# Kernel optimization log

Measured on AMD Instinct MI355X. Metric: run time of the kernel, lower is better.

Reference implementation:

```python
import jax, jax.numpy as jnp
import numpy as np

N = 2_000_000
WIDTH, HEIGHT = 1920, 1080
ZNEAR, ZFAR = 0.01, 100.0
TAN_FOVX = 0.5773503  # 60 deg horizontal FoV
TAN_FOVY = TAN_FOVX * HEIGHT / WIDTH


def _camera():
    # Row-vector convention: x_view = x_h @ world2view (translation in last row).
    w2v = np.eye(4, dtype=np.float32)
    w2v[3, 2] = 5.0  # push scene 5 units in front of the camera
    P = np.zeros((4, 4), dtype=np.float32)
    P[0, 0] = 1.0 / TAN_FOVX
    P[1, 1] = 1.0 / TAN_FOVY
    P[2, 2] = ZFAR / (ZFAR - ZNEAR)
    P[3, 2] = -(ZFAR * ZNEAR) / (ZFAR - ZNEAR)
    P[2, 3] = 1.0
    full = w2v @ P
    return jnp.asarray(w2v), jnp.asarray(full)


def setup_inputs() -> dict:
    key = jax.random.key(0)
    ks = jax.random.split(key, 5)
    w2v, full = _camera()
    return dict(
        points=jax.random.normal(ks[0], (N, 3), jnp.float32) * 2.0,
        colors=jax.random.uniform(ks[1], (N, 3), jnp.float32),
        opacity=jax.random.normal(ks[2], (N,), jnp.float32),
        scales=jax.random.uniform(ks[3], (N, 3), jnp.float32, minval=0.01, maxval=0.2),
        quaternions=jax.random.normal(ks[4], (N, 4), jnp.float32),
        world2view=w2v,
        full_proj_transform=full,
        tan_fovX=jnp.full((1,), TAN_FOVX, jnp.float32),
        tan_fovY=jnp.full((1,), TAN_FOVY, jnp.float32),
        focal_x=jnp.full((1,), WIDTH / (2.0 * TAN_FOVX), jnp.float32),
        focal_y=jnp.full((1,), HEIGHT / (2.0 * TAN_FOVY), jnp.float32),
        width=WIDTH,
        height=HEIGHT,
    )


def _quat_to_rot(q):
    q = q / jnp.linalg.norm(q, axis=-1, keepdims=True)
    w, x, y, z = q[:, 0], q[:, 1], q[:, 2], q[:, 3]
    R = jnp.stack([
        1 - 2 * (y * y + z * z), 2 * (x * y - w * z), 2 * (x * z + w * y),
        2 * (x * y + w * z), 1 - 2 * (x * x + z * z), 2 * (y * z - w * x),
        2 * (x * z - w * y), 2 * (y * z + w * x), 1 - 2 * (x * x + y * y),
    ], axis=-1)
    return R.reshape(-1, 3, 3)


def reference(points, colors, opacity, scales, quaternions, world2view,
              full_proj_transform, tan_fovX, tan_fovY, focal_x, focal_y,
              width, height):
    n = points.shape[0]
    # --- 3D covariance: Sigma = (R S)(R S)^T ---
    R = _quat_to_rot(quaternions)                      # [N,3,3]
    M = R * scales[:, None, :]                         # R @ diag(s)
    cov3d = jnp.einsum('nij,nkj->nik', M, M)           # [N,3,3]

    # --- view / clip transforms (row-vector convention) ---
    ph = jnp.concatenate([points, jnp.ones((n, 1), points.dtype)], axis=1)
    pview = ph @ world2view                            # [N,4]
    zview = pview[:, 2]
    in_view = zview >= 0.2                             # frustum (near-plane) cull

    pclip = ph @ full_proj_transform
    pndc = pclip[:, :3] / pclip[:, 3:4]
    px = ((pndc[:, 0] + 1.0) * width - 1.0) * 0.5      # ndc2Pix
    py = ((pndc[:, 1] + 1.0) * height - 1.0) * 0.5

    # --- 2D covariance via projection Jacobian (EWA splatting) ---
    xc = jnp.clip(pview[:, 0] / zview, -1.3 * tan_fovX, 1.3 * tan_fovX) * zview
    yc = jnp.clip(pview[:, 1] / zview, -1.3 * tan_fovY, 1.3 * tan_fovY) * zview
    z2 = zview * zview
    zero = jnp.zeros_like(zview)
    J = jnp.stack([
        focal_x / zview, zero, -(focal_x * xc) / z2,
        zero, focal_y / zview, -(focal_y * yc) / z2,
        zero, zero, zero,
    ], axis=-1).reshape(-1, 3, 3)                      # [N,3,3]
    W = world2view[:3, :3].T
    T = jnp.einsum('nij,jk->nik', J, W)
    cov2d = jnp.einsum('nij,njk,nlk->nil', T, cov3d, T)[:, :2, :2]

    # --- analytic 2x2 inverse ---
    c00, c01 = cov2d[:, 0, 0], cov2d[:, 0, 1]
    c10, c11 = cov2d[:, 1, 0], cov2d[:, 1, 1]
    det = c00 * c11 - c01 * c10
    det_safe = jnp.where(jnp.abs(det) < 1e-6, 1e-6, det)
    inv_cov = jnp.stack([c11, -c01, -c10, c00], axis=-1) / det_safe[:, None]

    # --- extent / radius: 3 sigma of dominant eigenvalue ---
    mid = 0.5 * (c00 + c11)
    inter = jnp.maximum(mid * mid - det, 0.1)
    lam = mid + jnp.sqrt(inter)
    radius = jnp.ceil(3.0 * jnp.sqrt(jnp.maximum(lam, 0.0)))

    min_x = jnp.floor(px - radius)
    min_y = jnp.floor(py - radius)
    max_x = jnp.ceil(px + radius)
    max_y = jnp.ceil(py + radius)

    # --- depth sort; culled gaussians keyed to +inf (fixed-shape stand-in for boolean gather) ---
    depth_key = jnp.where(in_view, zview, jnp.float32(jnp.inf))
    order = jnp.argsort(depth_key)

    packed = jnp.concatenate([
        px[:, None], py[:, None], zview[:, None],
        cov2d.reshape(n, 4), inv_cov,
        radius[:, None],
        min_x[:, None], min_y[:, None], max_x[:, None], max_y[:, None],
        colors, jax.nn.sigmoid(opacity)[:, None],
        in_view.astype(points.dtype)[:, None],
    ], axis=1)                                          # [N,21]
    return packed[order]
```

## Files before the change

kernel.cpp:

```cpp
#include <hip/hip_runtime.h>
#include <hip/hip_bf16.h>
#include <math.h>

#define BLK   256
#define IPT   16
#define TILE  (BLK * IPT)
#define CHUNK 1024
#define BINS  256
#define PASSES 4
#define SCT   4096

__global__ __launch_bounds__(256) void k_rows(const float* __restrict__ pts,
                                              const float* __restrict__ cols,
                                              const float* __restrict__ opa,
                                              const float* __restrict__ scl,
                                              const float* __restrict__ qt,
                                              const float* __restrict__ w2v,
                                              const float* __restrict__ fpm,
                                              const float* __restrict__ tanx_p,
                                              const float* __restrict__ tany_p,
                                              const float* __restrict__ fx_p,
                                              const float* __restrict__ fy_p,
                                              const int* __restrict__ wp,
                                              const int* __restrict__ hp,
                                              float* __restrict__ rows,
                                              unsigned* __restrict__ keys,
                                              int N)
{
    int i = blockIdx.x * 256 + threadIdx.x;
    if (i >= N) return;

    float x = pts[3*i+0], y = pts[3*i+1], z = pts[3*i+2];

    float zv = x*w2v[2] + y*w2v[6] + z*w2v[10] + w2v[14];
    bool in_view = (zv >= 0.2f);
    {
        float key = in_view ? zv : __int_as_float(0x7f800000);
        unsigned u = __float_as_uint(key);
        u ^= (u & 0x80000000u) ? 0xFFFFFFFFu : 0x80000000u;
        keys[i] = u;
    }

    float4 q4 = *(const float4*)(qt + 4*i);
    float qw = q4.x, qx = q4.y, qy = q4.z, qz = q4.w;
    float rn = __builtin_amdgcn_rsqf(qw*qw + qx*qx + qy*qy + qz*qz);
    qw *= rn; qx *= rn; qy *= rn; qz *= rn;
    float R00 = 1.f - 2.f*(qy*qy + qz*qz), R01 = 2.f*(qx*qy - qw*qz), R02 = 2.f*(qx*qz + qw*qy);
    float R10 = 2.f*(qx*qy + qw*qz), R11 = 1.f - 2.f*(qx*qx + qz*qz), R12 = 2.f*(qy*qz - qw*qx);
    float R20 = 2.f*(qx*qz - qw*qy), R21 = 2.f*(qy*qz + qw*qx), R22 = 1.f - 2.f*(qx*qx + qy*qy);

    float s0 = scl[3*i+0], s1 = scl[3*i+1], s2 = scl[3*i+2];
    float M00=R00*s0, M01=R01*s1, M02=R02*s2;
    float M10=R10*s0, M11=R11*s1, M12=R12*s2;
    float M20=R20*s0, M21=R21*s1, M22=R22*s2;
    float C00=M00*M00+M01*M01+M02*M02;
    float C01=M00*M10+M01*M11+M02*M12;
    float C02=M00*M20+M01*M21+M02*M22;
    float C11=M10*M10+M11*M11+M12*M12;
    float C12=M10*M20+M11*M21+M12*M22;
    float C22=M20*M20+M21*M21+M22*M22;

    float pvx = x*w2v[0] + y*w2v[4] + z*w2v[8]  + w2v[12];
    float pvy = x*w2v[1] + y*w2v[5] + z*w2v[9]  + w2v[13];

    float cx = x*fpm[0] + y*fpm[4] + z*fpm[8]  + fpm[12];
    float cy = x*fpm[1] + y*fpm[5] + z*fpm[9]  + fpm[13];
    float cw = x*fpm[3] + y*fpm[7] + z*fpm[11] + fpm[15];
    float rcw = __builtin_amdgcn_rcpf(cw);
    float Wf = (float)wp[0], Hf = (float)hp[0];
    float px = ((cx*rcw + 1.f) * Wf - 1.f) * 0.5f;
    float py = ((cy*rcw + 1.f) * Hf - 1.f) * 0.5f;

    float tanX = tanx_p[0], tanY = tany_p[0], fx = fx_p[0], fy = fy_p[0];
    float lx = 1.3f * tanX, ly = 1.3f * tanY;
    float rzv = __builtin_amdgcn_rcpf(zv);
    float xc = fminf(fmaxf(pvx*rzv, -lx), lx) * zv;
    float yc = fminf(fmaxf(pvy*rzv, -ly), ly) * zv;
    float rz2 = rzv * rzv;
    float J00 = fx * rzv, J02 = -(fx * xc) * rz2;
    float J11 = fy * rzv, J12 = -(fy * yc) * rz2;

    float T00 = J00*w2v[0] + J02*w2v[2];
    float T01 = J00*w2v[4] + J02*w2v[6];
    float T02 = J00*w2v[8] + J02*w2v[10];
    float T10 = J11*w2v[1] + J12*w2v[2];
    float T11 = J11*w2v[5] + J12*w2v[6];
    float T12 = J11*w2v[9] + J12*w2v[10];

    float V00 = T00*C00 + T01*C01 + T02*C02;
    float V01 = T00*C01 + T01*C11 + T02*C12;
    float V02 = T00*C02 + T01*C12 + T02*C22;
    float V10 = T10*C00 + T11*C01 + T12*C02;
    float V11 = T10*C01 + T11*C11 + T12*C12;
    float V12 = T10*C02 + T11*C12 + T12*C22;
    float c00 = V00*T00 + V01*T01 + V02*T02;
    float c01 = V00*T10 + V01*T11 + V02*T12;
    float c10 = V10*T00 + V11*T01 + V12*T02;
    float c11 = V10*T10 + V11*T11 + V12*T12;

    float det = c00*c11 - c01*c10;
    float det_safe = (fabsf(det) < 1e-6f) ? 1e-6f : det;
    float rdet = __builtin_amdgcn_rcpf(det_safe);
    float i00 =  c11 * rdet, i01 = -c01 * rdet, i11 = c00 * rdet;
    float mid = 0.5f * (c00 + c11);
    float inter = fmaxf(mid*mid - det, 0.1f);
    float lam = mid + sqrtf(inter);
    float radius = ceilf(3.0f * sqrtf(fmaxf(lam, 0.0f)));
    float op = __builtin_amdgcn_rcpf(1.0f + __expf(-opa[i]));

    float cr = cols[3*i+0], cg = cols[3*i+1], cb = cols[3*i+2];

    float4* rp = (float4*)(rows + (size_t)i * 16);
    rp[0] = make_float4(px,  py,  zv,  c00);
    rp[1] = make_float4(c01, c11, i00, i01);
    rp[2] = make_float4(i11, radius, cr, cg);
    rp[3] = make_float4(cb,  op,  in_view ? 1.0f : 0.0f, 0.f);
}

__global__ __launch_bounds__(256) void k_hist8(const unsigned* __restrict__ keys,
                                               int N, int numTiles, int shift,
                                               unsigned* __restrict__ hist)
{
    __shared__ unsigned hb[4][BINS];
    int t = threadIdx.x, b = blockIdx.x, w = t >> 6;
    hb[0][t] = 0; hb[1][t] = 0; hb[2][t] = 0; hb[3][t] = 0;
    __syncthreads();
    int base = b * TILE + t * 16;
    if (base + 16 <= N) {
        const uint4* p = (const uint4*)(keys + base);
        #pragma unroll
        for (int q = 0; q < 4; ++q) {
            uint4 v = p[q];
            atomicAdd(&hb[w][(v.x >> shift) & 255u], 1u);
            atomicAdd(&hb[w][(v.y >> shift) & 255u], 1u);
            atomicAdd(&hb[w][(v.z >> shift) & 255u], 1u);
            atomicAdd(&hb[w][(v.w >> shift) & 255u], 1u);
        }
    } else {
        for (int k = 0; k < 16; ++k) {
            int i = base + k;
            if (i < N) atomicAdd(&hb[w][(keys[i] >> shift) & 255u], 1u);
        }
    }
    __syncthreads();
    hist[t * numTiles + b] = hb[0][t] + hb[1][t] + hb[2][t] + hb[3][t];
}

__global__ __launch_bounds__(256) void k_scanA(const unsigned* __restrict__ h, int E,
                                               unsigned* __restrict__ bsum)
{
    __shared__ unsigned red[256];
    int t = threadIdx.x;
    int base = blockIdx.x * SCT + t * 16;
    unsigned acc = 0;
    if (base + 16 <= E) {
        const uint4* p = (const uint4*)(h + base);
        #pragma unroll
        for (int q = 0; q < 4; ++q) { uint4 v = p[q]; acc += v.x + v.y + v.z + v.w; }
    } else {
        for (int k = 0; k < 16; ++k) { int i = base + k; if (i < E) acc += h[i]; }
    }
    red[t] = acc;
    __syncthreads();
    for (int off = 128; off > 0; off >>= 1) {
        if (t < off) red[t] += red[t + off];
        __syncthreads();
    }
    if (t == 0) bsum[blockIdx.x] = red[0];
}

__global__ __launch_bounds__(256) void k_scanB(unsigned* __restrict__ h, int E,
                                               const unsigned* __restrict__ bsum)
{
    __shared__ unsigned tsum[256];
    __shared__ unsigned boff_s;
    int t = threadIdx.x, b = blockIdx.x;
    int base = b * SCT + t * 16;

    if (t == 0) { unsigned o = 0; for (int i = 0; i < b; ++i) o += bsum[i]; boff_s = o; }

    unsigned v[16];
    bool full = (base + 16 <= E);
    if (full) {
        const uint4* p = (const uint4*)(h + base);
        #pragma unroll
        for (int q = 0; q < 4; ++q) { uint4 u = p[q]; v[4*q]=u.x; v[4*q+1]=u.y; v[4*q+2]=u.z; v[4*q+3]=u.w; }
    } else {
        for (int k = 0; k < 16; ++k) { int i = base + k; v[k] = (i < E) ? h[i] : 0u; }
    }
    unsigned acc = 0;
    #pragma unroll
    for (int k = 0; k < 16; ++k) { unsigned x = v[k]; v[k] = acc; acc += x; }
    tsum[t] = acc;
    __syncthreads();
    for (int off = 1; off < 256; off <<= 1) {
        unsigned u = (t >= off) ? tsum[t - off] : 0u;
        __syncthreads();
        tsum[t] += u;
        __syncthreads();
    }
    unsigned add = boff_s + ((t == 0) ? 0u : tsum[t - 1]);
    if (full) {
        uint4* p = (uint4*)(h + base);
        #pragma unroll
        for (int q = 0; q < 4; ++q)
            p[q] = make_uint4(v[4*q] + add, v[4*q+1] + add, v[4*q+2] + add, v[4*q+3] + add);
    } else {
        for (int k = 0; k < 16; ++k) { int i = base + k; if (i < E) h[i] = v[k] + add; }
    }
}

__global__ __launch_bounds__(256) void k_scatter8(const unsigned* __restrict__ keys,
                                                  const unsigned* __restrict__ vals,
                                                  int N, int numTiles, int shift,
                                                  const unsigned* __restrict__ hist,
                                                  unsigned* __restrict__ okeys,
                                                  unsigned* __restrict__ ovals)
{
    __shared__ unsigned short wcnt[4][BINS];
    __shared__ unsigned digStartL[BINS];
    __shared__ unsigned tileBase[BINS];
    __shared__ unsigned tscan[BINS];
    __shared__ unsigned stage[TILE];

    int t = threadIdx.x, b = blockIdx.x;
    int w = t >> 6, l = t & 63;
    int base = b * TILE;
    int nvalid = N - base; if (nvalid < 0) nvalid = 0; if (nvalid > TILE) nvalid = TILE;
    int wbase = base + w * CHUNK;

    ((unsigned*)wcnt)[t] = 0; ((unsigned*)wcnt)[256 + t] = 0;
    __syncthreads();

    unsigned k_[IPT];
    unsigned short rw_[IPT];
    unsigned char d_[IPT];

    #pragma unroll
    for (int it = 0; it < IPT; ++it) {
        int e = wbase + it * 64 + l;
        bool ok = e < N;
        unsigned kk = ok ? keys[e] : 0u;
        unsigned d = (kk >> shift) & 255u;
        unsigned long long mm = __ballot(ok);
        #pragma unroll
        for (int bb = 0; bb < 8; ++bb) {
            unsigned long long bal = __ballot(ok && ((d >> bb) & 1u));
            mm &= ((d >> bb) & 1u) ? bal : ~bal;
        }
        unsigned long long below = mm & ((1ull << l) - 1ull);
        unsigned rk = (unsigned)__popcll(below);
        unsigned before = (unsigned)wcnt[w][d];
        if (ok && rk == 0)
            wcnt[w][d] = (unsigned short)(before + (unsigned)__popcll(mm));
        k_[it]  = kk;
        rw_[it] = (unsigned short)(before + rk);
        d_[it]  = (unsigned char)d;
    }
    __syncthreads();

    {
        unsigned c0 = wcnt[0][t], c1 = wcnt[1][t], c2 = wcnt[2][t], c3 = wcnt[3][t];
        wcnt[0][t] = 0;
        wcnt[1][t] = (unsigned short)c0;
        wcnt[2][t] = (unsigned short)(c0 + c1);
        wcnt[3][t] = (unsigned short)(c0 + c1 + c2);
        tscan[t] = c0 + c1 + c2 + c3;
        tileBase[t] = hist[t * numTiles + b];
    }
    __syncthreads();
    for (int off = 1; off < 256; off <<= 1) {
        unsigned u = (t >= off) ? tscan[t - off] : 0u;
        __syncthreads();
        tscan[t] += u;
        __syncthreads();
    }
    digStartL[t] = (t == 0) ? 0u : tscan[t - 1];
    __syncthreads();

    unsigned lp_[IPT];
    #pragma unroll
    for (int it = 0; it < IPT; ++it) {
        int e = wbase + it * 64 + l;
        if (e < N) {
            unsigned d = d_[it];
            lp_[it] = digStartL[d] + (unsigned)wcnt[w][d] + (unsigned)rw_[it];
            stage[lp_[it]] = k_[it];
        }
    }
    __syncthreads();

    unsigned pos_[IPT];
    #pragma unroll
    for (int it = 0; it < IPT; ++it) {
        int p = it * BLK + t;
        if (p < nvalid) {
            unsigned kk = stage[p];
            unsigned d = (kk >> shift) & 255u;
            unsigned pos = tileBase[d] + ((unsigned)p - digStartL[d]);
            pos_[it] = pos;
            if (okeys) okeys[pos] = kk;
        }
    }
    __syncthreads();

    #pragma unroll
    for (int it = 0; it < IPT; ++it) {
        int e = wbase + it * 64 + l;
        if (e < N) stage[lp_[it]] = vals ? vals[e] : (unsigned)e;
    }
    __syncthreads();
    #pragma unroll
    for (int it = 0; it < IPT; ++it) {
        int p = it * BLK + t;
        if (p < nvalid) ovals[pos_[it]] = stage[p];
    }
}

__global__ __launch_bounds__(256) void k_perm(const unsigned* __restrict__ order,
                                              const float* __restrict__ rows,
                                              float* __restrict__ out, int N)
{
    __shared__ float srow[256 * 21];
    int i = blockIdx.x * 256 + threadIdx.x;
    if (i < N) {
        int j = (int)order[i];
        const float4* rp = (const float4*)(rows + (size_t)j * 16);
        float4 a = rp[0], b4 = rp[1], c4 = rp[2], d4 = rp[3];
        float px = a.x,  py = a.y,  zv = a.z,  c00 = a.w;
        float c01 = b4.x, c11 = b4.y, i00 = b4.z, i01 = b4.w;
        float i11 = c4.x, rad = c4.y, cr = c4.z, cg = c4.w;
        float cb = d4.x,  op = d4.y,  iv = d4.z;
        float* r = &srow[threadIdx.x * 21];
        r[0]=px; r[1]=py; r[2]=zv;
        r[3]=c00; r[4]=c01; r[5]=c01; r[6]=c11;
        r[7]=i00; r[8]=i01; r[9]=i01; r[10]=i11;
        r[11]=rad;
        r[12]=floorf(px - rad); r[13]=floorf(py - rad);
        r[14]=ceilf(px + rad);  r[15]=ceilf(py + rad);
        r[16]=cr; r[17]=cg; r[18]=cb;
        r[19]=op; r[20]=iv;
    }
    __syncthreads();
    int blockBase = blockIdx.x * 256;
    int valid = N - blockBase; if (valid > 256) valid = 256;
    if (valid > 0) {
        float* dst = out + (size_t)blockBase * 21;
        for (int u = threadIdx.x; u < valid * 21; u += 256) dst[u] = srow[u];
    }
}

extern "C" void kernel_launch(void* const* d_in, const int* in_sizes, int n_in,
                              void* d_out, int out_size, void* d_ws, size_t ws_size,
                              hipStream_t stream)
{
    const float* pts  = (const float*)d_in[0];
    const float* cols = (const float*)d_in[1];
    const float* opa  = (const float*)d_in[2];
    const float* scl  = (const float*)d_in[3];
    const float* qt   = (const float*)d_in[4];
    const float* w2v  = (const float*)d_in[5];
    const float* fpm  = (const float*)d_in[6];
    const float* tanx = (const float*)d_in[7];
    const float* tany = (const float*)d_in[8];
    const float* fx   = (const float*)d_in[9];
    const float* fy   = (const float*)d_in[10];
    const int*   wp   = (const int*)d_in[11];
    const int*   hp   = (const int*)d_in[12];

    int N = in_sizes[0] / 3;
    int numTiles = (N + TILE - 1) / TILE;
    int nb = (N + 255) / 256;
    int E = BINS * numTiles;
    int nScan = (E + SCT - 1) / SCT;

    unsigned* kA   = (unsigned*)d_ws;
    unsigned* kB   = kA + N;
    unsigned* vA   = kB + N;
    unsigned* vB   = vA + N;
    unsigned* hist = vB + N;
    unsigned* bsum = hist + E;
    float*    rows = (float*)(bsum + nScan);

    k_rows<<<nb, 256, 0, stream>>>(pts, cols, opa, scl, qt, w2v, fpm,
                                   tanx, tany, fx, fy, wp, hp, rows, kA, N);

    k_hist8<<<numTiles, 256, 0, stream>>>(kA, N, numTiles, 0, hist);
    k_scanA<<<nScan, 256, 0, stream>>>(hist, E, bsum);
    k_scanB<<<nScan, 256, 0, stream>>>(hist, E, bsum);
    k_scatter8<<<numTiles, 256, 0, stream>>>(kA, nullptr, N, numTiles, 0, hist, kB, vA);

    k_hist8<<<numTiles, 256, 0, stream>>>(kB, N, numTiles, 8, hist);
    k_scanA<<<nScan, 256, 0, stream>>>(hist, E, bsum);
    k_scanB<<<nScan, 256, 0, stream>>>(hist, E, bsum);
    k_scatter8<<<numTiles, 256, 0, stream>>>(kB, vA, N, numTiles, 8, hist, kA, vB);

    k_hist8<<<numTiles, 256, 0, stream>>>(kA, N, numTiles, 16, hist);
    k_scanA<<<nScan, 256, 0, stream>>>(hist, E, bsum);
    k_scanB<<<nScan, 256, 0, stream>>>(hist, E, bsum);
    k_scatter8<<<numTiles, 256, 0, stream>>>(kA, vB, N, numTiles, 16, hist, kB, vA);

    k_hist8<<<numTiles, 256, 0, stream>>>(kB, N, numTiles, 24, hist);
    k_scanA<<<nScan, 256, 0, stream>>>(hist, E, bsum);
    k_scanB<<<nScan, 256, 0, stream>>>(hist, E, bsum);
    k_scatter8<<<numTiles, 256, 0, stream>>>(kB, vA, N, numTiles, 24, hist, nullptr, vB);

    k_perm<<<nb, 256, 0, stream>>>(vB, rows, (float*)d_out, N);
}
```

Measured before the change: 503.4 us.

## Replace per-pass histogram/scan with one-sweep histogram and decoupled look-back scatter

Computes all four 8-bit digit histograms in a single pass over the keys, using wave-level match aggregation, then scans them in one small kernel. Each scatter pass then derives its per-tile digit offsets with a decoupled look-back over tile states. Tiles are ordered by an atomic ticket so that waiting on predecessors is safe. This removes three histogram passes and eight scan launches, plus the per-tile histogram traffic. In exchange it adds a zeroing kernel and spin-waiting between tiles.

```diff
diff --git a/kernel.cpp b/kernel.cpp
--- a/kernel.cpp
+++ b/kernel.cpp
@@ -1,14 +1,22 @@
 #include <hip/hip_runtime.h>
-#include <hip/hip_bf16.h>
 #include <math.h>
 
 #define BLK   256
 #define IPT   16
-#define TILE  (BLK * IPT)
+#define TILE  4096
 #define CHUNK 1024
 #define BINS  256
-#define PASSES 4
-#define SCT   4096
+
+#define FLAG_AGG (1u << 30)
+#define FLAG_PRE (2u << 30)
+#define VALMASK  0x3FFFFFFFu
+
+__global__ __launch_bounds__(256) void k_zero(unsigned* __restrict__ p, int n)
+{
+    int i = blockIdx.x * 256 + threadIdx.x;
+    int T = gridDim.x * 256;
+    for (; i < n; i += T) p[i] = 0;
+}
 
 __global__ __launch_bounds__(256) void k_rows(const float* __restrict__ pts,
                                               const float* __restrict__ cols,
@@ -117,120 +125,96 @@
     rp[3] = make_float4(cb,  op,  in_view ? 1.0f : 0.0f, 0.f);
 }
 
-__global__ __launch_bounds__(256) void k_hist8(const unsigned* __restrict__ keys,
-                                               int N, int numTiles, int shift,
-                                               unsigned* __restrict__ hist)
+__global__ __launch_bounds__(256) void k_hist_all(const unsigned* __restrict__ keys,
+                                                  int N, unsigned* __restrict__ gh)
 {
     __shared__ unsigned hb[4][BINS];
-    int t = threadIdx.x, b = blockIdx.x, w = t >> 6;
+    int t = threadIdx.x, l = t & 63;
     hb[0][t] = 0; hb[1][t] = 0; hb[2][t] = 0; hb[3][t] = 0;
     __syncthreads();
-    int base = b * TILE + t * 16;
-    if (base + 16 <= N) {
-        const uint4* p = (const uint4*)(keys + base);
+
+    int gtid = blockIdx.x * 256 + t;
+    int T = gridDim.x * 256;
+    int M4 = N >> 2;
+    for (int i = gtid; i < M4; i += T) {
+        uint4 v = ((const uint4*)keys)[i];
+        unsigned ks[4] = {v.x, v.y, v.z, v.w};
         #pragma unroll
-        for (int q = 0; q < 4; ++q) {
-            uint4 v = p[q];
-            atomicAdd(&hb[w][(v.x >> shift) & 255u], 1u);
-            atomicAdd(&hb[w][(v.y >> shift) & 255u], 1u);
-            atomicAdd(&hb[w][(v.z >> shift) & 255u], 1u);
-            atomicAdd(&hb[w][(v.w >> shift) & 255u], 1u);
-        }
-    } else {
-        for (int k = 0; k < 16; ++k) {
-            int i = base + k;
-            if (i < N) atomicAdd(&hb[w][(keys[i] >> shift) & 255u], 1u);
-        }
-    }
-    __syncthreads();
-    hist[t * numTiles + b] = hb[0][t] + hb[1][t] + hb[2][t] + hb[3][t];
-}
-
-__global__ __launch_bounds__(256) void k_scanA(const unsigned* __restrict__ h, int E,
-                                               unsigned* __restrict__ bsum)
-{
-    __shared__ unsigned red[256];
+        for (int c = 0; c < 4; ++c) {
+            unsigned kk = ks[c];
+            #pragma unroll
+            for (int p = 0; p < 4; ++p) {
+                unsigned d = (kk >> (8*p)) & 255u;
+                unsigned long long mm = __ballot(true);
+                #pragma unroll
+                for (int bb = 0; bb < 8; ++bb) {
+                    unsigned long long bal = __ballot(((d >> bb) & 1u) != 0u);
+                    mm &= ((d >> bb) & 1u) ? bal : ~bal;
+                }
+                unsigned long long below = mm & ((1ull << l) - 1ull);
+                if (below == 0ull)
+                    atomicAdd(&hb[p][d], (unsigned)__popcll(mm));
+            }
+        }
+    }
+    if (gtid == 0) {
+        for (int i = M4 << 2; i < N; ++i) {
+            unsigned kk = keys[i];
+            for (int p = 0; p < 4; ++p) atomicAdd(&hb[p][(kk >> (8*p)) & 255u], 1u);
+        }
+    }
+    __syncthreads();
+    #pragma unroll
+    for (int p = 0; p < 4; ++p)
+        if (hb[p][t]) atomicAdd(&gh[p * BINS + t], hb[p][t]);
+}
+
+__global__ __launch_bounds__(256) void k_scan_all(unsigned* __restrict__ gh)
+{
+    __shared__ unsigned tsum[BINS];
     int t = threadIdx.x;
-    int base = blockIdx.x * SCT + t * 16;
-    unsigned acc = 0;
-    if (base + 16 <= E) {
-        const uint4* p = (const uint4*)(h + base);
-        #pragma unroll
-        for (int q = 0; q < 4; ++q) { uint4 v = p[q]; acc += v.x + v.y + v.z + v.w; }
-    } else {
-        for (int k = 0; k < 16; ++k) { int i = base + k; if (i < E) acc += h[i]; }
-    }
-    red[t] = acc;
-    __syncthreads();
-    for (int off = 128; off > 0; off >>= 1) {
-        if (t < off) red[t] += red[t + off];
+    for (int p = 0; p < 4; ++p) {
+        tsum[t] = gh[p * BINS + t];
         __syncthreads();
-    }
-    if (t == 0) bsum[blockIdx.x] = red[0];
-}
-
-__global__ __launch_bounds__(256) void k_scanB(unsigned* __restrict__ h, int E,
-                                               const unsigned* __restrict__ bsum)
-{
-    __shared__ unsigned tsum[256];
-    __shared__ unsigned boff_s;
-    int t = threadIdx.x, b = blockIdx.x;
-    int base = b * SCT + t * 16;
-
-    if (t == 0) { unsigned o = 0; for (int i = 0; i < b; ++i) o += bsum[i]; boff_s = o; }
-
-    unsigned v[16];
-    bool full = (base + 16 <= E);
-    if (full) {
-        const uint4* p = (const uint4*)(h + base);
-        #pragma unroll
-        for (int q = 0; q < 4; ++q) { uint4 u = p[q]; v[4*q]=u.x; v[4*q+1]=u.y; v[4*q+2]=u.z; v[4*q+3]=u.w; }
-    } else {
-        for (int k = 0; k < 16; ++k) { int i = base + k; v[k] = (i < E) ? h[i] : 0u; }
-    }
-    unsigned acc = 0;
-    #pragma unroll
-    for (int k = 0; k < 16; ++k) { unsigned x = v[k]; v[k] = acc; acc += x; }
-    tsum[t] = acc;
-    __syncthreads();
-    for (int off = 1; off < 256; off <<= 1) {
-        unsigned u = (t >= off) ? tsum[t - off] : 0u;
+        for (int off = 1; off < 256; off <<= 1) {
+            unsigned u = (t >= off) ? tsum[t - off] : 0u;
+            __syncthreads();
+            tsum[t] += u;
+            __syncthreads();
+        }
+        unsigned excl = (t == 0) ? 0u : tsum[t - 1];
         __syncthreads();
-        tsum[t] += u;
+        gh[p * BINS + t] = excl;
         __syncthreads();
     }
-    unsigned add = boff_s + ((t == 0) ? 0u : tsum[t - 1]);
-    if (full) {
-        uint4* p = (uint4*)(h + base);
-        #pragma unroll
-        for (int q = 0; q < 4; ++q)
-            p[q] = make_uint4(v[4*q] + add, v[4*q+1] + add, v[4*q+2] + add, v[4*q+3] + add);
-    } else {
-        for (int k = 0; k < 16; ++k) { int i = base + k; if (i < E) h[i] = v[k] + add; }
-    }
-}
-
-__global__ __launch_bounds__(256) void k_scatter8(const unsigned* __restrict__ keys,
-                                                  const unsigned* __restrict__ vals,
-                                                  int N, int numTiles, int shift,
-                                                  const unsigned* __restrict__ hist,
-                                                  unsigned* __restrict__ okeys,
-                                                  unsigned* __restrict__ ovals)
+}
+
+__global__ __launch_bounds__(256) void k_scatter_lb(const unsigned* __restrict__ keys,
+                                                    const unsigned* __restrict__ vals,
+                                                    int N, int shift,
+                                                    const unsigned* __restrict__ gbase,
+                                                    unsigned* __restrict__ tstate,
+                                                    unsigned* __restrict__ ticket,
+                                                    unsigned* __restrict__ okeys,
+                                                    unsigned* __restrict__ ovals)
 {
     __shared__ unsigned short wcnt[4][BINS];
     __shared__ unsigned digStartL[BINS];
     __shared__ unsigned tileBase[BINS];
     __shared__ unsigned tscan[BINS];
     __shared__ unsigned stage[TILE];
-
-    int t = threadIdx.x, b = blockIdx.x;
+    __shared__ unsigned vt_s;
+
+    int t = threadIdx.x;
+    if (t == 0) vt_s = atomicAdd(ticket, 1u);
+    ((unsigned*)wcnt)[t] = 0; ((unsigned*)wcnt)[256 + t] = 0;
+    __syncthreads();
+
+    int b = (int)vt_s;
     int w = t >> 6, l = t & 63;
     int base = b * TILE;
     int nvalid = N - base; if (nvalid < 0) nvalid = 0; if (nvalid > TILE) nvalid = TILE;
     int wbase = base + w * CHUNK;
-
-    ((unsigned*)wcnt)[t] = 0; ((unsigned*)wcnt)[256 + t] = 0;
-    __syncthreads();
 
     unsigned k_[IPT];
     unsigned short rw_[IPT];
@@ -259,14 +243,17 @@
     }
     __syncthreads();
 
+    unsigned own;
     {
         unsigned c0 = wcnt[0][t], c1 = wcnt[1][t], c2 = wcnt[2][t], c3 = wcnt[3][t];
         wcnt[0][t] = 0;
         wcnt[1][t] = (unsigned short)c0;
         wcnt[2][t] = (unsigned short)(c0 + c1);
         wcnt[3][t] = (unsigned short)(c0 + c1 + c2);
-        tscan[t] = c0 + c1 + c2 + c3;
-        tileBase[t] = hist[t * numTiles + b];
+        own = c0 + c1 + c2 + c3;
+        tscan[t] = own;
+        __hip_atomic_store(&tstate[(size_t)b * BINS + t], FLAG_AGG | own,
+                           __ATOMIC_RELEASE, __HIP_MEMORY_SCOPE_AGENT);
     }
     __syncthreads();
     for (int off = 1; off < 256; off <<= 1) {
@@ -276,6 +263,25 @@
         __syncthreads();
     }
     digStartL[t] = (t == 0) ? 0u : tscan[t - 1];
+
+    {
+        unsigned sum = 0;
+        int p = b - 1;
+        while (p >= 0) {
+            unsigned s;
+            do {
+                s = __hip_atomic_load(&tstate[(size_t)p * BINS + t],
+                                      __ATOMIC_RELAXED, __HIP_MEMORY_SCOPE_AGENT);
+                if ((s >> 30) == 0u) __builtin_amdgcn_s_sleep(1);
+            } while ((s >> 30) == 0u);
+            sum += s & VALMASK;
+            if (s & FLAG_PRE) break;
+            --p;
+        }
+        tileBase[t] = gbase[t] + sum;
+        __hip_atomic_store(&tstate[(size_t)b * BINS + t], FLAG_PRE | (sum + own),
+                           __ATOMIC_RELEASE, __HIP_MEMORY_SCOPE_AGENT);
+    }
     __syncthreads();
 
     unsigned lp_[IPT];
@@ -371,39 +377,33 @@
     int N = in_sizes[0] / 3;
     int numTiles = (N + TILE - 1) / TILE;
     int nb = (N + 255) / 256;
-    int E = BINS * numTiles;
-    int nScan = (E + SCT - 1) / SCT;
-
-    unsigned* kA   = (unsigned*)d_ws;
-    unsigned* kB   = kA + N;
-    unsigned* vA   = kB + N;
-    unsigned* vB   = vA + N;
-    unsigned* hist = vB + N;
-    unsigned* bsum = hist + E;
-    float*    rows = (float*)(bsum + nScan);
-
+
+    unsigned* kA     = (unsigned*)d_ws;
+    unsigned* kB     = kA + N;
+    unsigned* vA     = kB + N;
+    unsigned* vB     = vA + N;
+    unsigned* gh     = vB + N;
+    unsigned* tick   = gh + 4 * BINS;
+    unsigned* tstate = tick + 4;
+    float*    rows   = (float*)(tstate + (size_t)4 * numTiles * BINS);
+
+    int zwords = 4 * BINS + 4 + 4 * numTiles * BINS;
+    int zb = (zwords + 255) / 256; if (zb > 1024) zb = 1024;
+
+    k_zero<<<zb, 256, 0, stream>>>(gh, zwords);
     k_rows<<<nb, 256, 0, stream>>>(pts, cols, opa, scl, qt, w2v, fpm,
                                    tanx, tany, fx, fy, wp, hp, rows, kA, N);
-
-    k_hist8<<<numTiles, 256, 0, stream>>>(kA, N, numTiles, 0, hist);
-    k_scanA<<<nScan, 256, 0, stream>>>(hist, E, bsum);
-    k_scanB<<<nScan, 256, 0, stream>>>(hist, E, bsum);
-    k_scatter8<<<numTiles, 256, 0, stream>>>(kA, nullptr, N, numTiles, 0, hist, kB, vA);
-
-    k_hist8<<<numTiles, 256, 0, stream>>>(kB, N, numTiles, 8, hist);
-    k_scanA<<<nScan, 256, 0, stream>>>(hist, E, bsum);
-    k_scanB<<<nScan, 256, 0, stream>>>(hist, E, bsum);
-    k_scatter8<<<numTiles, 256, 0, stream>>>(kB, vA, N, numTiles, 8, hist, kA, vB);
-
-    k_hist8<<<numTiles, 256, 0, stream>>>(kA, N, numTiles, 16, hist);
-    k_scanA<<<nScan, 256, 0, stream>>>(hist, E, bsum);
-    k_scanB<<<nScan, 256, 0, stream>>>(hist, E, bsum);
-    k_scatter8<<<numTiles, 256, 0, stream>>>(kA, vB, N, numTiles, 16, hist, kB, vA);
-
-    k_hist8<<<numTiles, 256, 0, stream>>>(kB, N, numTiles, 24, hist);
-    k_scanA<<<nScan, 256, 0, stream>>>(hist, E, bsum);
-    k_scanB<<<nScan, 256, 0, stream>>>(hist, E, bsum);
-    k_scatter8<<<numTiles, 256, 0, stream>>>(kB, vA, N, numTiles, 24, hist, nullptr, vB);
+    k_hist_all<<<512, 256, 0, stream>>>(kA, N, gh);
+    k_scan_all<<<1, 256, 0, stream>>>(gh);
+
+    k_scatter_lb<<<numTiles, 256, 0, stream>>>(kA, nullptr, N, 0,  gh + 0*BINS,
+                                               tstate + (size_t)0*numTiles*BINS, tick + 0, kB, vA);
+    k_scatter_lb<<<numTiles, 256, 0, stream>>>(kB, vA, N, 8,  gh + 1*BINS,
+                                               tstate + (size_t)1*numTiles*BINS, tick + 1, kA, vB);
+    k_scatter_lb<<<numTiles, 256, 0, stream>>>(kA, vB, N, 16, gh + 2*BINS,
+                                               tstate + (size_t)2*numTiles*BINS, tick + 2, kB, vA);
+    k_scatter_lb<<<numTiles, 256, 0, stream>>>(kB, vA, N, 24, gh + 3*BINS,
+                                               tstate + (size_t)3*numTiles*BINS, tick + 3, nullptr, vB);
 
     k_perm<<<nb, 256, 0, stream>>>(vB, rows, (float*)d_out, N);
 }
```

After: 843.7 us. 1.68x slower.

## Fuse radix histograms into rows and scatter kernels, halve tile size

Applied to the files above, without the earlier changes.

Removes the four standalone histogram kernels. The first-digit histogram is built inside the preprocessing kernel, and each later pass's histogram is accumulated in the previous scatter through global atomics keyed by output tile. Tile size drops from 4096 to 2048 keys, which doubles the histogram size, and four histogram buffers plus a zeroing kernel are added. This saves three full key reads and launches, at the cost of many scattered global atomics in the scatter kernel.

```diff
diff --git a/kernel.cpp b/kernel.cpp
--- a/kernel.cpp
+++ b/kernel.cpp
@@ -1,14 +1,20 @@
 #include <hip/hip_runtime.h>
-#include <hip/hip_bf16.h>
 #include <math.h>
 
 #define BLK   256
-#define IPT   16
-#define TILE  (BLK * IPT)
-#define CHUNK 1024
+#define IPT   8
+#define TILE  2048
+#define TSHIFT 11
+#define CHUNK 512
 #define BINS  256
-#define PASSES 4
 #define SCT   4096
+
+__global__ __launch_bounds__(256) void k_zero(unsigned* __restrict__ p, int n)
+{
+    int i = blockIdx.x * 256 + threadIdx.x;
+    int T = gridDim.x * 256;
+    for (; i < n; i += T) p[i] = 0;
+}
 
 __global__ __launch_bounds__(256) void k_rows(const float* __restrict__ pts,
                                               const float* __restrict__ cols,
@@ -25,125 +31,107 @@
                                               const int* __restrict__ hp,
                                               float* __restrict__ rows,
                                               unsigned* __restrict__ keys,
-                                              int N)
-{
-    int i = blockIdx.x * 256 + threadIdx.x;
-    if (i >= N) return;
-
-    float x = pts[3*i+0], y = pts[3*i+1], z = pts[3*i+2];
-
-    float zv = x*w2v[2] + y*w2v[6] + z*w2v[10] + w2v[14];
-    bool in_view = (zv >= 0.2f);
-    {
-        float key = in_view ? zv : __int_as_float(0x7f800000);
-        unsigned u = __float_as_uint(key);
-        u ^= (u & 0x80000000u) ? 0xFFFFFFFFu : 0x80000000u;
-        keys[i] = u;
-    }
-
-    float4 q4 = *(const float4*)(qt + 4*i);
-    float qw = q4.x, qx = q4.y, qy = q4.z, qz = q4.w;
-    float rn = __builtin_amdgcn_rsqf(qw*qw + qx*qx + qy*qy + qz*qz);
-    qw *= rn; qx *= rn; qy *= rn; qz *= rn;
-    float R00 = 1.f - 2.f*(qy*qy + qz*qz), R01 = 2.f*(qx*qy - qw*qz), R02 = 2.f*(qx*qz + qw*qy);
-    float R10 = 2.f*(qx*qy + qw*qz), R11 = 1.f - 2.f*(qx*qx + qz*qz), R12 = 2.f*(qy*qz - qw*qx);
-    float R20 = 2.f*(qx*qz - qw*qy), R21 = 2.f*(qy*qz + qw*qx), R22 = 1.f - 2.f*(qx*qx + qy*qy);
-
-    float s0 = scl[3*i+0], s1 = scl[3*i+1], s2 = scl[3*i+2];
-    float M00=R00*s0, M01=R01*s1, M02=R02*s2;
-    float M10=R10*s0, M11=R11*s1, M12=R12*s2;
-    float M20=R20*s0, M21=R21*s1, M22=R22*s2;
-    float C00=M00*M00+M01*M01+M02*M02;
-    float C01=M00*M10+M01*M11+M02*M12;
-    float C02=M00*M20+M01*M21+M02*M22;
-    float C11=M10*M10+M11*M11+M12*M12;
-    float C12=M10*M20+M11*M21+M12*M22;
-    float C22=M20*M20+M21*M21+M22*M22;
-
-    float pvx = x*w2v[0] + y*w2v[4] + z*w2v[8]  + w2v[12];
-    float pvy = x*w2v[1] + y*w2v[5] + z*w2v[9]  + w2v[13];
-
-    float cx = x*fpm[0] + y*fpm[4] + z*fpm[8]  + fpm[12];
-    float cy = x*fpm[1] + y*fpm[5] + z*fpm[9]  + fpm[13];
-    float cw = x*fpm[3] + y*fpm[7] + z*fpm[11] + fpm[15];
-    float rcw = __builtin_amdgcn_rcpf(cw);
-    float Wf = (float)wp[0], Hf = (float)hp[0];
-    float px = ((cx*rcw + 1.f) * Wf - 1.f) * 0.5f;
-    float py = ((cy*rcw + 1.f) * Hf - 1.f) * 0.5f;
-
-    float tanX = tanx_p[0], tanY = tany_p[0], fx = fx_p[0], fy = fy_p[0];
-    float lx = 1.3f * tanX, ly = 1.3f * tanY;
-    float rzv = __builtin_amdgcn_rcpf(zv);
-    float xc = fminf(fmaxf(pvx*rzv, -lx), lx) * zv;
-    float yc = fminf(fmaxf(pvy*rzv, -ly), ly) * zv;
-    float rz2 = rzv * rzv;
-    float J00 = fx * rzv, J02 = -(fx * xc) * rz2;
-    float J11 = fy * rzv, J12 = -(fy * yc) * rz2;
-
-    float T00 = J00*w2v[0] + J02*w2v[2];
-    float T01 = J00*w2v[4] + J02*w2v[6];
-    float T02 = J00*w2v[8] + J02*w2v[10];
-    float T10 = J11*w2v[1] + J12*w2v[2];
-    float T11 = J11*w2v[5] + J12*w2v[6];
-    float T12 = J11*w2v[9] + J12*w2v[10];
-
-    float V00 = T00*C00 + T01*C01 + T02*C02;
-    float V01 = T00*C01 + T01*C11 + T02*C12;
-    float V02 = T00*C02 + T01*C12 + T02*C22;
-    float V10 = T10*C00 + T11*C01 + T12*C02;
-    float V11 = T10*C01 + T11*C11 + T12*C12;
-    float V12 = T10*C02 + T11*C12 + T12*C22;
-    float c00 = V00*T00 + V01*T01 + V02*T02;
-    float c01 = V00*T10 + V01*T11 + V02*T12;
-    float c10 = V10*T00 + V11*T01 + V12*T02;
-    float c11 = V10*T10 + V11*T11 + V12*T12;
-
-    float det = c00*c11 - c01*c10;
-    float det_safe = (fabsf(det) < 1e-6f) ? 1e-6f : det;
-    float rdet = __builtin_amdgcn_rcpf(det_safe);
-    float i00 =  c11 * rdet, i01 = -c01 * rdet, i11 = c00 * rdet;
-    float mid = 0.5f * (c00 + c11);
-    float inter = fmaxf(mid*mid - det, 0.1f);
-    float lam = mid + sqrtf(inter);
-    float radius = ceilf(3.0f * sqrtf(fmaxf(lam, 0.0f)));
-    float op = __builtin_amdgcn_rcpf(1.0f + __expf(-opa[i]));
-
-    float cr = cols[3*i+0], cg = cols[3*i+1], cb = cols[3*i+2];
-
-    float4* rp = (float4*)(rows + (size_t)i * 16);
-    rp[0] = make_float4(px,  py,  zv,  c00);
-    rp[1] = make_float4(c01, c11, i00, i01);
-    rp[2] = make_float4(i11, radius, cr, cg);
-    rp[3] = make_float4(cb,  op,  in_view ? 1.0f : 0.0f, 0.f);
-}
-
-__global__ __launch_bounds__(256) void k_hist8(const unsigned* __restrict__ keys,
-                                               int N, int numTiles, int shift,
-                                               unsigned* __restrict__ hist)
-{
-    __shared__ unsigned hb[4][BINS];
-    int t = threadIdx.x, b = blockIdx.x, w = t >> 6;
-    hb[0][t] = 0; hb[1][t] = 0; hb[2][t] = 0; hb[3][t] = 0;
-    __syncthreads();
-    int base = b * TILE + t * 16;
-    if (base + 16 <= N) {
-        const uint4* p = (const uint4*)(keys + base);
-        #pragma unroll
-        for (int q = 0; q < 4; ++q) {
-            uint4 v = p[q];
-            atomicAdd(&hb[w][(v.x >> shift) & 255u], 1u);
-            atomicAdd(&hb[w][(v.y >> shift) & 255u], 1u);
-            atomicAdd(&hb[w][(v.z >> shift) & 255u], 1u);
-            atomicAdd(&hb[w][(v.w >> shift) & 255u], 1u);
+                                              unsigned* __restrict__ hist0,
+                                              int numTiles, int N)
+{
+    __shared__ unsigned hcnt[BINS];
+    int t = threadIdx.x;
+    hcnt[t] = 0;
+    __syncthreads();
+
+    int i = blockIdx.x * 256 + t;
+    if (i < N) {
+        float x = pts[3*i+0], y = pts[3*i+1], z = pts[3*i+2];
+
+        float zv = x*w2v[2] + y*w2v[6] + z*w2v[10] + w2v[14];
+        bool in_view = (zv >= 0.2f);
+        unsigned u;
+        {
+            float key = in_view ? zv : __int_as_float(0x7f800000);
+            u = __float_as_uint(key);
+            u ^= (u & 0x80000000u) ? 0xFFFFFFFFu : 0x80000000u;
+            keys[i] = u;
         }
-    } else {
-        for (int k = 0; k < 16; ++k) {
-            int i = base + k;
-            if (i < N) atomicAdd(&hb[w][(keys[i] >> shift) & 255u], 1u);
-        }
-    }
-    __syncthreads();
-    hist[t * numTiles + b] = hb[0][t] + hb[1][t] + hb[2][t] + hb[3][t];
+        atomicAdd(&hcnt[u & 255u], 1u);
+
+        float4 q4 = *(const float4*)(qt + 4*i);
+        float qw = q4.x, qx = q4.y, qy = q4.z, qz = q4.w;
+        float rn = __builtin_amdgcn_rsqf(qw*qw + qx*qx + qy*qy + qz*qz);
+        qw *= rn; qx *= rn; qy *= rn; qz *= rn;
+        float R00 = 1.f - 2.f*(qy*qy + qz*qz), R01 = 2.f*(qx*qy - qw*qz), R02 = 2.f*(qx*qz + qw*qy);
+        float R10 = 2.f*(qx*qy + qw*qz), R11 = 1.f - 2.f*(qx*qx + qz*qz), R12 = 2.f*(qy*qz - qw*qx);
+        float R20 = 2.f*(qx*qz - qw*qy), R21 = 2.f*(qy*qz + qw*qx), R22 = 1.f - 2.f*(qx*qx + qy*qy);
+
+        float s0 = scl[3*i+0], s1 = scl[3*i+1], s2 = scl[3*i+2];
+        float M00=R00*s0, M01=R01*s1, M02=R02*s2;
+        float M10=R10*s0, M11=R11*s1, M12=R12*s2;
+        float M20=R20*s0, M21=R21*s1, M22=R22*s2;
+        float C00=M00*M00+M01*M01+M02*M02;
+        float C01=M00*M10+M01*M11+M02*M12;
+        float C02=M00*M20+M01*M21+M02*M22;
+        float C11=M10*M10+M11*M11+M12*M12;
+        float C12=M10*M20+M11*M21+M12*M22;
+        float C22=M20*M20+M21*M21+M22*M22;
+
+        float pvx = x*w2v[0] + y*w2v[4] + z*w2v[8]  + w2v[12];
+        float pvy = x*w2v[1] + y*w2v[5] + z*w2v[9]  + w2v[13];
+
+        float cx = x*fpm[0] + y*fpm[4] + z*fpm[8]  + fpm[12];
+        float cy = x*fpm[1] + y*fpm[5] + z*fpm[9]  + fpm[13];
+        float cw = x*fpm[3] + y*fpm[7] + z*fpm[11] + fpm[15];
+        float rcw = __builtin_amdgcn_rcpf(cw);
+        float Wf = (float)wp[0], Hf = (float)hp[0];
+        float px = ((cx*rcw + 1.f) * Wf - 1.f) * 0.5f;
+        float py = ((cy*rcw + 1.f) * Hf - 1.f) * 0.5f;
+
+        float tanX = tanx_p[0], tanY = tany_p[0], fx = fx_p[0], fy = fy_p[0];
+        float lx = 1.3f * tanX, ly = 1.3f * tanY;
+        float rzv = __builtin_amdgcn_rcpf(zv);
+        float xc = fminf(fmaxf(pvx*rzv, -lx), lx) * zv;
+        float yc = fminf(fmaxf(pvy*rzv, -ly), ly) * zv;
+        float rz2 = rzv * rzv;
+        float J00 = fx * rzv, J02 = -(fx * xc) * rz2;
+        float J11 = fy * rzv, J12 = -(fy * yc) * rz2;
+
+        float T00 = J00*w2v[0] + J02*w2v[2];
+        float T01 = J00*w2v[4] + J02*w2v[6];
+        float T02 = J00*w2v[8] + J02*w2v[10];
+        float T10 = J11*w2v[1] + J12*w2v[2];
+        float T11 = J11*w2v[5] + J12*w2v[6];
+        float T12 = J11*w2v[9] + J12*w2v[10];
+
+        float V00 = T00*C00 + T01*C01 + T02*C02;
+        float V01 = T00*C01 + T01*C11 + T02*C12;
+        float V02 = T00*C02 + T01*C12 + T02*C22;
+        float V10 = T10*C00 + T11*C01 + T12*C02;
+        float V11 = T10*C01 + T11*C11 + T12*C12;
+        float V12 = T10*C02 + T11*C12 + T12*C22;
+        float c00 = V00*T00 + V01*T01 + V02*T02;
+        float c01 = V00*T10 + V01*T11 + V02*T12;
+        float c10 = V10*T00 + V11*T01 + V12*T02;
+        float c11 = V10*T10 + V11*T11 + V12*T12;
+
+        float det = c00*c11 - c01*c10;
+        float det_safe = (fabsf(det) < 1e-6f) ? 1e-6f : det;
+        float rdet = __builtin_amdgcn_rcpf(det_safe);
+        float i00 =  c11 * rdet, i01 = -c01 * rdet, i11 = c00 * rdet;
+        float mid = 0.5f * (c00 + c11);
+        float inter = fmaxf(mid*mid - det, 0.1f);
+        float lam = mid + sqrtf(inter);
+        float radius = ceilf(3.0f * sqrtf(fmaxf(lam, 0.0f)));
+        float op = __builtin_amdgcn_rcpf(1.0f + __expf(-opa[i]));
+
+        float cr = cols[3*i+0], cg = cols[3*i+1], cb = cols[3*i+2];
+
+        float4* rp = (float4*)(rows + (size_t)i * 16);
+        rp[0] = make_float4(px,  py,  zv,  c00);
+        rp[1] = make_float4(c01, c11, i00, i01);
+        rp[2] = make_float4(i11, radius, cr, cg);
+        rp[3] = make_float4(cb,  op,  in_view ? 1.0f : 0.0f, 0.f);
+    }
+    __syncthreads();
+    int tile0 = (blockIdx.x * 256) >> TSHIFT;
+    if (hcnt[t]) atomicAdd(&hist0[t * numTiles + tile0], hcnt[t]);
 }
 
 __global__ __launch_bounds__(256) void k_scanA(const unsigned* __restrict__ h, int E,
@@ -214,6 +202,8 @@
                                                   const unsigned* __restrict__ vals,
                                                   int N, int numTiles, int shift,
                                                   const unsigned* __restrict__ hist,
+                                                  unsigned* __restrict__ histNext,
+                                                  int nextShift,
                                                   unsigned* __restrict__ okeys,
                                                   unsigned* __restrict__ ovals)
 {
@@ -300,6 +290,10 @@
             unsigned pos = tileBase[d] + ((unsigned)p - digStartL[d]);
             pos_[it] = pos;
             if (okeys) okeys[pos] = kk;
+            if (histNext) {
+                unsigned d2 = (kk >> nextShift) & 255u;
+                atomicAdd(&histNext[d2 * numTiles + (pos >> TSHIFT)], 1u);
+            }
         }
     }
     __syncthreads();
@@ -378,32 +372,38 @@
     unsigned* kB   = kA + N;
     unsigned* vA   = kB + N;
     unsigned* vB   = vA + N;
-    unsigned* hist = vB + N;
-    unsigned* bsum = hist + E;
+    unsigned* h0   = vB + N;
+    unsigned* h1   = h0 + E;
+    unsigned* h2   = h1 + E;
+    unsigned* h3   = h2 + E;
+    unsigned* bsum = h3 + E;
     float*    rows = (float*)(bsum + nScan);
 
+    {
+        int zwords = 4 * E;
+        int zb = (zwords + 255) / 256; if (zb > 1024) zb = 1024;
+        k_zero<<<zb, 256, 0, stream>>>(h0, zwords);
+    }
+
     k_rows<<<nb, 256, 0, stream>>>(pts, cols, opa, scl, qt, w2v, fpm,
-                                   tanx, tany, fx, fy, wp, hp, rows, kA, N);
-
-    k_hist8<<<numTiles, 256, 0, stream>>>(kA, N, numTiles, 0, hist);
-    k_scanA<<<nScan, 256, 0, stream>>>(hist, E, bsum);
-    k_scanB<<<nScan, 256, 0, stream>>>(hist, E, bsum);
-    k_scatter8<<<numTiles, 256, 0, stream>>>(kA, nullptr, N, numTiles, 0, hist, kB, vA);
-
-    k_hist8<<<numTiles, 256, 0, stream>>>(kB, N, numTiles, 8, hist);
-    k_scanA<<<nScan, 256, 0, stream>>>(hist, E, bsum);
-    k_scanB<<<nScan, 256, 0, stream>>>(hist, E, bsum);
-    k_scatter8<<<numTiles, 256, 0, stream>>>(kB, vA, N, numTiles, 8, hist, kA, vB);
-
-    k_hist8<<<numTiles, 256, 0, stream>>>(kA, N, numTiles, 16, hist);
-    k_scanA<<<nScan, 256, 0, stream>>>(hist, E, bsum);
-    k_scanB<<<nScan, 256, 0, stream>>>(hist, E, bsum);
-    k_scatter8<<<numTiles, 256, 0, stream>>>(kA, vB, N, numTiles, 16, hist, kB, vA);
-
-    k_hist8<<<numTiles, 256, 0, stream>>>(kB, N, numTiles, 24, hist);
-    k_scanA<<<nScan, 256, 0, stream>>>(hist, E, bsum);
-    k_scanB<<<nScan, 256, 0, stream>>>(hist, E, bsum);
-    k_scatter8<<<numTiles, 256, 0, stream>>>(kB, vA, N, numTiles, 24, hist, nullptr, vB);
+                                   tanx, tany, fx, fy, wp, hp, rows, kA,
+                                   h0, numTiles, N);
+
+    k_scanA<<<nScan, 256, 0, stream>>>(h0, E, bsum);
+    k_scanB<<<nScan, 256, 0, stream>>>(h0, E, bsum);
+    k_scatter8<<<numTiles, 256, 0, stream>>>(kA, nullptr, N, numTiles, 0,  h0, h1, 8,  kB, vA);
+
+    k_scanA<<<nScan, 256, 0, stream>>>(h1, E, bsum);
+    k_scanB<<<nScan, 256, 0, stream>>>(h1, E, bsum);
+    k_scatter8<<<numTiles, 256, 0, stream>>>(kB, vA, N, numTiles, 8,  h1, h2, 16, kA, vB);
+
+    k_scanA<<<nScan, 256, 0, stream>>>(h2, E, bsum);
+    k_scanB<<<nScan, 256, 0, stream>>>(h2, E, bsum);
+    k_scatter8<<<numTiles, 256, 0, stream>>>(kA, vB, N, numTiles, 16, h2, h3, 24, kB, vA);
+
+    k_scanA<<<nScan, 256, 0, stream>>>(h3, E, bsum);
+    k_scanB<<<nScan, 256, 0, stream>>>(h3, E, bsum);
+    k_scatter8<<<numTiles, 256, 0, stream>>>(kB, vA, N, numTiles, 24, h3, nullptr, 0, nullptr, vB);
 
     k_perm<<<nb, 256, 0, stream>>>(vB, rows, (float*)d_out, N);
 }
```

After: 1.452 ms. +188.4%, slower.
